# Kernel optimization log

Measured on AMD Instinct MI355X. Metric: run time of the kernel, lower is better.

The kernel has to match this reference:

```python
import math
import jax, jax.numpy as jnp
import numpy as np

NUM_BUCKETS = 32
MAX_DISTANCE = 128
N_HEADS = 16
D_KV = 64


def _relative_position_bucket(rel_pos):
    # encoder (bidirectional) path of UMT5Attention._relative_position_bucket
    num_buckets = NUM_BUCKETS // 2
    rel_buckets = (rel_pos > 0).astype(jnp.int32) * num_buckets
    rel_pos = jnp.abs(rel_pos)
    max_exact = num_buckets // 2
    is_small = rel_pos < max_exact
    # clamp to 1 inside log only to avoid nan; those entries are masked by is_small
    rel_pos_large = max_exact + (
        jnp.log(jnp.maximum(rel_pos, 1).astype(jnp.float32) / max_exact)
        / math.log(MAX_DISTANCE / max_exact)
        * (num_buckets - max_exact)
    ).astype(jnp.int32)
    rel_pos_large = jnp.minimum(rel_pos_large, num_buckets - 1)
    return rel_buckets + jnp.where(is_small, rel_pos, rel_pos_large)


def compute_bias(rel_bias, q_len, k_len):
    ctx = jnp.arange(q_len, dtype=jnp.int32)[:, None]
    mem = jnp.arange(k_len, dtype=jnp.int32)[None, :]
    bkt = _relative_position_bucket(mem - ctx)          # [q, k]
    values = rel_bias[bkt]                               # [q, k, H]
    return jnp.transpose(values, (2, 0, 1))[None]        # [1, H, q, k]


def setup_inputs() -> dict:
    key = jax.random.key(0)
    ks = jax.random.split(key, 6)
    B, S, D = 2, 2048, 1024
    s = 1.0 / math.sqrt(D)
    return {
        "hidden_states": jax.random.normal(ks[0], (B, S, D), jnp.float32),
        "attention_mask": jnp.ones((B, S), jnp.int32),
        "Wq": jax.random.normal(ks[1], (D, D), jnp.float32) * s,
        "Wk": jax.random.normal(ks[2], (D, D), jnp.float32) * s,
        "Wv": jax.random.normal(ks[3], (D, D), jnp.float32) * s,
        "Wo": jax.random.normal(ks[4], (D, D), jnp.float32) * s,
        "rel_bias": jax.random.normal(ks[5], (NUM_BUCKETS, N_HEADS), jnp.float32),
    }


def reference(hidden_states, attention_mask, Wq, Wk, Wv, Wo, rel_bias):
    b, s, _ = hidden_states.shape
    n, c = N_HEADS, D_KV
    q = (hidden_states @ Wq).reshape(b, s, n, c)
    k = (hidden_states @ Wk).reshape(b, s, n, c)
    v = (hidden_states @ Wv).reshape(b, s, n, c)
    position_bias = compute_bias(rel_bias, s, s)          # [1, H, s, s]
    mask = attention_mask[:, None, None, :]               # [b, 1, 1, s]
    position_bias = jnp.where(mask == 0,
                              jnp.finfo(hidden_states.dtype).min,
                              position_bias)
    # T5-style: no 1/sqrt(d) query scaling
    attn = jnp.einsum('binc,bjnc->bnij', q, k) + position_bias
    attn = jax.nn.softmax(attn, axis=-1)
    o = jnp.einsum('bnij,bjnc->binc', attn, v).reshape(b, s, n * c)
    return o @ Wo
```

## Files before the change

### kernel.cpp

```cpp
#include <hip/hip_runtime.h>
#include <hip/hip_bf16.h>

#define NH 16
#define DC 64
#define SEQ 2048
#define BATCH 2
#define DM 1024
#define MTOT (BATCH*SEQ)

#define LOG2E 1.44269504f
#define SMAX_BOUND 48.0f

typedef unsigned short u16;
typedef unsigned int u32;
typedef __bf16 bf16x8 __attribute__((ext_vector_type(8)));
typedef float f32x4 __attribute__((ext_vector_type(4)));
typedef int i32x4 __attribute__((ext_vector_type(4)));
typedef unsigned u32x2v __attribute__((ext_vector_type(2)));

struct __attribute__((packed, aligned(4))) f4u { f32x4 v; };

__device__ __forceinline__ u16 f2bf(float f) {
    unsigned int x = __float_as_uint(f);
    unsigned int r = (x + 0x7fffu + ((x >> 16) & 1u)) >> 16;
    return (u16)r;
}
__device__ __forceinline__ u32 cvtpk(float a, float b) {
    u32 r;
    asm("v_cvt_pk_bf16_f32 %0, %1, %2" : "=v"(r) : "v"(a), "v"(b));
    return r;
}

__device__ __forceinline__ float fexp2(float x) {
#if __has_builtin(__builtin_amdgcn_exp2f)
    return __builtin_amdgcn_exp2f(x);
#else
    return exp2f(x);
#endif
}

__device__ __forceinline__ f32x4 mfma16(bf16x8 a, bf16x8 b, f32x4 c) {
    return __builtin_amdgcn_mfma_f32_16x16x32_bf16(a, b, c, 0, 0, 0);
}

__device__ __forceinline__ void glds(const u16* g, u16* l) {
    __builtin_amdgcn_global_load_lds(
        (const __attribute__((address_space(1))) void*)g,
        (__attribute__((address_space(3))) void*)l, 16, 0, 0);
}

__device__ __forceinline__ float psum32(float v) {
    u32x2v t = __builtin_amdgcn_permlane32_swap(__float_as_uint(v), __float_as_uint(v), false, false);
    return __uint_as_float(t.x) + __uint_as_float(t.y);
}
__device__ __forceinline__ float psum16(float v) {
    u32x2v t = __builtin_amdgcn_permlane16_swap(__float_as_uint(v), __float_as_uint(v), false, false);
    return __uint_as_float(t.x) + __uint_as_float(t.y);
}


__global__ __launch_bounds__(256) void prep_kernel(
    const float* __restrict__ hs,
    const float* __restrict__ Wq, const float* __restrict__ Wk,
    const float* __restrict__ Wv, const float* __restrict__ Wo,
    const float* __restrict__ rel_bias,
    u16* __restrict__ hsb, u16* __restrict__ wT, float* __restrict__ btab)
{
    int bid = blockIdx.x, tid = threadIdx.x;
    if (bid < 4096) {
        int z = bid >> 10, rem = bid & 1023;
        int by = rem >> 5, bx = rem & 31;
        const float* W = (z == 0) ? Wq : (z == 1) ? Wk : (z == 2) ? Wv : Wo;
        float sc = (z == 0) ? LOG2E : 1.0f;
        u16* WT = wT + (size_t)z * DM * DM;
        __shared__ float tile[32][33];
        int tx = tid & 31, ty = tid >> 5;
        int kbase = by * 32, nbase = bx * 32;
#pragma unroll
        for (int i = 0; i < 4; i++)
            tile[ty * 4 + i][tx] = W[(size_t)(kbase + ty * 4 + i) * DM + nbase + tx];
        __syncthreads();
#pragma unroll
        for (int i = 0; i < 4; i++)
            WT[(size_t)(nbase + ty * 4 + i) * DM + kbase + tx] = f2bf(tile[tx][ty * 4 + i] * sc);
    } else if (bid < 6144) {
        int idx = (bid - 4096) * 256 + tid;
        int stride = 2048 * 256;
        int n4 = MTOT * DM / 4;
        for (int i = idx; i < n4; i += stride) {
            float4 v = reinterpret_cast<const float4*>(hs)[i];
            uint2 o;
            o.x = (unsigned)f2bf(v.x) | ((unsigned)f2bf(v.y) << 16);
            o.y = (unsigned)f2bf(v.z) | ((unsigned)f2bf(v.w) << 16);
            reinterpret_cast<uint2*>(hsb)[i] = o;
        }
    } else {
        int idx = (bid - 6144) * 256 + tid;
        int n = idx >> 12;
        int dpos = idx & 4095;
        int delta = dpos - 2048;
        int rb = (delta > 0) ? 16 : 0;
        int a = (delta < 0) ? -delta : delta;
        int ib;
        if (a < 8) {
            ib = a;
        } else {
            ib = 8 + (int)(logf((float)a / 8.0f) / logf(16.0f) * 8.0f);
            if (ib > 15) ib = 15;
        }
        btab[idx] = (rel_bias[(rb + ib) * NH + n] - SMAX_BOUND) * LOG2E;
    }
}

__global__ __launch_bounds__(256) void vtrans(const u16* __restrict__ V, u16* __restrict__ VT) {
    int st = blockIdx.x;
    int hb = blockIdx.y;
    const u16* src = V + ((size_t)hb * SEQ + st * 64) * DC;
    u16* dst = VT + (size_t)hb * DC * SEQ + st * 64;
    __shared__ u16 t[64][65];
    int tid = threadIdx.x;
    int r = tid >> 2, c0 = (tid & 3) * 16;
    union { bf16x8 v; u16 s[8]; } a0, a1;
    a0.v = *reinterpret_cast<const bf16x8*>(src + (size_t)r * DC + c0);
    a1.v = *reinterpret_cast<const bf16x8*>(src + (size_t)r * DC + c0 + 8);
#pragma unroll
    for (int j = 0; j < 8; j++) { t[r][c0 + j] = a0.s[j]; t[r][c0 + 8 + j] = a1.s[j]; }
    __syncthreads();
    int c = tid >> 2, s0 = (tid & 3) * 16;
    union { bf16x8 v; u16 s[8]; } o0, o1;
#pragma unroll
    for (int j = 0; j < 8; j++) { o0.s[j] = t[s0 + j][c]; o1.s[j] = t[s0 + 8 + j][c]; }
    *reinterpret_cast<bf16x8*>(dst + (size_t)c * SEQ + s0)     = o0.v;
    *reinterpret_cast<bf16x8*>(dst + (size_t)c * SEQ + s0 + 8) = o1.v;
}


template<int MODE>
__global__ __launch_bounds__(256) void gemm_bt(
    const u16* __restrict__ A, const u16* __restrict__ BT,
    u16* __restrict__ qkvout, float* __restrict__ fout)
{
    const int NTILES = DM / 128;
    const int MTILES = MTOT / 128;
    __shared__ u16 As[128 * 32];
    __shared__ u16 Bs[128 * 32];

    int nb8 = gridDim.x >> 3;
    int bid = (blockIdx.x & 7) * nb8 + (blockIdx.x >> 3);

    int proj = 0, mt, nt;
    if (MODE == 0) {
        proj = bid / (MTILES * NTILES);
        int r = bid % (MTILES * NTILES);
        mt = r / NTILES; nt = r % NTILES;
    } else {
        mt = bid / NTILES; nt = bid % NTILES;
    }
    const u16* Bp = BT + (size_t)proj * DM * DM;
    int m0 = mt * 128, n0 = nt * 128;
    int tid = threadIdx.x;
    int lane = tid & 63, wid = tid >> 6;
    int wrow = (wid >> 1) * 64, wcol = (wid & 1) * 64;

    f32x4 acc[4][4] = {};

    int srow = lane >> 2;
    int skoff = (lane & 3) * 8;

    for (int k0 = 0; k0 < DM; k0 += 32) {
        __syncthreads();
#pragma unroll
        for (int t = 0; t < 2; t++) {
            int chunk = wid * 2 + t;
            int row = chunk * 16 + srow;
            glds(A + (size_t)(m0 + row) * DM + k0 + skoff, &As[chunk * 512]);
        }
#pragma unroll
        for (int t = 0; t < 2; t++) {
            int chunk = wid * 2 + t;
            int row = chunk * 16 + srow;
            glds(Bp + (size_t)(n0 + row) * DM + k0 + skoff, &Bs[chunk * 512]);
        }
        __syncthreads();

        int ko = (lane >> 4) * 8;
        bf16x8 af[4], bfr[4];
#pragma unroll
        for (int mi = 0; mi < 4; mi++)
            af[mi] = *reinterpret_cast<const bf16x8*>(&As[(wrow + mi * 16 + (lane & 15)) * 32 + ko]);
#pragma unroll
        for (int ni = 0; ni < 4; ni++)
            bfr[ni] = *reinterpret_cast<const bf16x8*>(&Bs[(wcol + ni * 16 + (lane & 15)) * 32 + ko]);
#pragma unroll
        for (int mi = 0; mi < 4; mi++)
#pragma unroll
            for (int ni = 0; ni < 4; ni++)
                acc[mi][ni] = mfma16(af[mi], bfr[ni], acc[mi][ni]);
    }

    int rbase = (lane >> 4) * 4;
    int cidx = lane & 15;
#pragma unroll
    for (int mi = 0; mi < 4; mi++) {
#pragma unroll
        for (int ni = 0; ni < 4; ni++) {
#pragma unroll
            for (int r = 0; r < 4; r++) {
                int gm = m0 + wrow + mi * 16 + rbase + r;
                int gn = n0 + wcol + ni * 16 + cidx;
                float v = acc[mi][ni][r];
                if (MODE == 0) {
                    int b = gm >> 11, s = gm & (SEQ - 1);
                    int h = gn >> 6, c = gn & 63;
                    size_t off = (((size_t)b * NH + h) * SEQ + s) * DC + c;
                    qkvout[(size_t)proj * MTOT * DM + off] = f2bf(v);
                } else {
                    fout[(size_t)gm * DM + gn] = v;
                }
            }
        }
    }
}


__global__ __launch_bounds__(512, 4) void attn_kernel(
    const u16* __restrict__ Q, const u16* __restrict__ K, const u16* __restrict__ VT,
    const int* __restrict__ mask, const float* __restrict__ btab,
    u16* __restrict__ O)
{
    __shared__ u16 smem[32768];
    __shared__ float lds_l[4][2][16];

    int wg = blockIdx.x;
    int sw = (wg & 7) * 64 + (wg >> 3);
    int qt = sw & 15;
    int bh = sw >> 4;
    int h = bh & 15, b = bh >> 4;

    int tid = threadIdx.x, lane = tid & 63, wid = tid >> 6;
    int q15 = lane & 15, hi = lane >> 4;
    int qg = wid >> 1, kh = wid & 1;

    const u16* Qp  = Q  + (((size_t)b * NH + h) * SEQ) * DC;
    const u16* Kp  = K  + (((size_t)b * NH + h) * SEQ) * DC;
    const u16* VTp = VT + ((size_t)b * NH + h) * DC * SEQ;

    int qb = qt * 128 + qg * 32;
    int iq0 = qb + q15;
    int iq1 = qb + 16 + q15;

    bf16x8 qf00 = *reinterpret_cast<const bf16x8*>(Qp + (size_t)iq0 * DC + hi * 8);
    bf16x8 qf01 = *reinterpret_cast<const bf16x8*>(Qp + (size_t)iq0 * DC + 32 + hi * 8);
    bf16x8 qf10 = *reinterpret_cast<const bf16x8*>(Qp + (size_t)iq1 * DC + hi * 8);
    bf16x8 qf11 = *reinterpret_cast<const bf16x8*>(Qp + (size_t)iq1 * DC + 32 + hi * 8);

    int c0 = wid * 2, c1 = wid * 2 + 1;
    int lr0 = (c0 & 7) * 8 + (lane >> 3);
    int lr1 = (c1 & 7) * 8 + (lane >> 3);
    int cc0 = (lane & 7) ^ (lr0 & 7);
    int cc1 = (lane & 7) ^ (lr1 & 7);
    const u16* g0 = (wid < 4) ? (Kp + (size_t)lr0 * DC + cc0 * 8)
                              : (VTp + (size_t)lr0 * SEQ + cc0 * 8);
    const u16* g1 = (wid < 4) ? (Kp + (size_t)lr1 * DC + cc1 * 8)
                              : (VTp + (size_t)lr1 * SEQ + cc1 * 8);
    int adv = (wid < 4) ? 64 * DC : 64;

    int x0 = (hi)         ^ (q15 & 7);
    int x1 = (hi + 4)     ^ (q15 & 7);
    int xv = (kh * 4 + hi) ^ (q15 & 7);

    const float* bp0 = btab + (size_t)h * 2 * SEQ + 2048 + kh * 32 + hi * 4 - iq0;
    const float* bp1 = bp0 - 16;
    const int* mkp = mask + (size_t)b * SEQ + kh * 32 + hi * 4;

    f32x4 lv0 = {}, lv1 = {};
    f32x4 oacc[4][2] = {};

    glds(g0, &smem[c0 * 512]);
    glds(g1, &smem[c1 * 512]);
    const u16* pg0 = g0 + adv;
    const u16* pg1 = g1 + adv;

#pragma unroll 2
    for (int t = 0; t < SEQ / 64; t++) {
        u16* KsT = smem + ((t & 3) << 13);
        u16* VsT = KsT + 4096;
        int kt = t * 64;

        f32x4 bvm0[2], bvm1[2];
#pragma unroll
        for (int kf = 0; kf < 2; kf++) {
            f32x4 bv0 = reinterpret_cast<const f4u*>(bp0 + kt + kf * 16)->v;
            f32x4 bv1 = reinterpret_cast<const f4u*>(bp1 + kt + kf * 16)->v;
            i32x4 mv4 = *reinterpret_cast<const i32x4*>(mkp + kt + kf * 16);
#pragma unroll
            for (int r = 0; r < 4; r++) {
                bool mv = (mv4[r] != 0);
                bvm0[kf][r] = mv ? bv0[r] : -1e30f;
                bvm1[kf][r] = mv ? bv1[r] : -1e30f;
            }
        }

        if (t < SEQ / 64 - 1) {
            u16* nb = smem + (((t + 1) & 3) << 13);
            glds(pg0, &nb[c0 * 512]);
            glds(pg1, &nb[c1 * 512]);
            pg0 += adv;
            pg1 += adv;
            asm volatile("s_waitcnt vmcnt(2)" ::: "memory");
        } else {
            asm volatile("s_waitcnt vmcnt(0)" ::: "memory");
        }
        asm volatile("s_barrier" ::: "memory");

        f32x4 s0[2], s1[2];
        __builtin_amdgcn_s_setprio(1);
#pragma unroll
        for (int kf = 0; kf < 2; kf++) {
            int row = ((kh * 2 + kf) * 16 + q15) * 64;
            bf16x8 ka0 = *reinterpret_cast<const bf16x8*>(&KsT[row + x0 * 8]);
            bf16x8 ka1 = *reinterpret_cast<const bf16x8*>(&KsT[row + x1 * 8]);
            f32x4 z0 = bvm0[kf];
            z0 = mfma16(ka0, qf00, z0);
            z0 = mfma16(ka1, qf01, z0);
            s0[kf] = z0;
            f32x4 z1 = bvm1[kf];
            z1 = mfma16(ka0, qf10, z1);
            z1 = mfma16(ka1, qf11, z1);
            s1[kf] = z1;
        }
        __builtin_amdgcn_s_setprio(0);

#pragma unroll
        for (int kf = 0; kf < 2; kf++) {
#pragma unroll
            for (int r = 0; r < 4; r++) {
                s0[kf][r] = fexp2(s0[kf][r]);
                s1[kf][r] = fexp2(s1[kf][r]);
            }
            lv0 += s0[kf];
            lv1 += s1[kf];
        }

        bf16x8 pa0, pa1;
        {
            u32 cA0 = cvtpk(s0[0][0], s0[0][1]);
            u32 cA1 = cvtpk(s0[0][2], s0[0][3]);
            u32 cB0 = cvtpk(s0[1][0], s0[1][1]);
            u32 cB1 = cvtpk(s0[1][2], s0[1][3]);
            u32x2v t0 = __builtin_amdgcn_permlane32_swap(cA0, cB0, false, false);
            u32x2v t1 = __builtin_amdgcn_permlane32_swap(cA1, cB1, false, false);
            u32x2v t2 = __builtin_amdgcn_permlane16_swap(t0.x, t0.y, false, false);
            u32x2v t3 = __builtin_amdgcn_permlane16_swap(t1.x, t1.y, false, false);
            union { u32 w[4]; bf16x8 v; } up;
            up.w[0] = t2.x; up.w[1] = t3.x; up.w[2] = t2.y; up.w[3] = t3.y;
            pa0 = up.v;
        }
        {
            u32 cA0 = cvtpk(s1[0][0], s1[0][1]);
            u32 cA1 = cvtpk(s1[0][2], s1[0][3]);
            u32 cB0 = cvtpk(s1[1][0], s1[1][1]);
            u32 cB1 = cvtpk(s1[1][2], s1[1][3]);
            u32x2v t0 = __builtin_amdgcn_permlane32_swap(cA0, cB0, false, false);
            u32x2v t1 = __builtin_amdgcn_permlane32_swap(cA1, cB1, false, false);
            u32x2v t2 = __builtin_amdgcn_permlane16_swap(t0.x, t0.y, false, false);
            u32x2v t3 = __builtin_amdgcn_permlane16_swap(t1.x, t1.y, false, false);
            union { u32 w[4]; bf16x8 v; } up;
            up.w[0] = t2.x; up.w[1] = t3.x; up.w[2] = t2.y; up.w[3] = t3.y;
            pa1 = up.v;
        }

        __builtin_amdgcn_s_setprio(1);
#pragma unroll
        for (int ci = 0; ci < 4; ci++) {
            bf16x8 vf = *reinterpret_cast<const bf16x8*>(&VsT[(ci * 16 + q15) * 64 + xv * 8]);
            oacc[ci][0] = mfma16(vf, pa0, oacc[ci][0]);
            oacc[ci][1] = mfma16(vf, pa1, oacc[ci][1]);
        }
        __builtin_amdgcn_s_setprio(0);
    }

    float l0 = (lv0[0] + lv0[1]) + (lv0[2] + lv0[3]);
    float l1 = (lv1[0] + lv1[1]) + (lv1[2] + lv1[3]);
    l0 = psum16(psum32(l0));
    l1 = psum16(psum32(l1));
    __syncthreads();

    float* fs = reinterpret_cast<float*>(smem);
    if (kh == 1) {
#pragma unroll
        for (int ci = 0; ci < 4; ci++)
#pragma unroll
            for (int qs = 0; qs < 2; qs++)
                *reinterpret_cast<f32x4*>(&fs[qg * 2048 + (ci * 2 + qs) * 256 + lane * 4]) = oacc[ci][qs];
        if (hi == 0) { lds_l[qg][0][q15] = l0; lds_l[qg][1][q15] = l1; }
    }
    __syncthreads();

    float rl0 = 0.0f, rl1 = 0.0f;
    if (kh == 0) {
#pragma unroll
        for (int ci = 0; ci < 4; ci++)
#pragma unroll
            for (int qs = 0; qs < 2; qs++)
                oacc[ci][qs] += *reinterpret_cast<const f32x4*>(&fs[qg * 2048 + (ci * 2 + qs) * 256 + lane * 4]);
        rl0 = 1.0f / (l0 + lds_l[qg][0][q15]);
        rl1 = 1.0f / (l1 + lds_l[qg][1][q15]);
    }
    __syncthreads();

    u16* Ot = smem;
    if (kh == 0) {
#pragma unroll
        for (int ci = 0; ci < 4; ci++) {
            u32 w00 = cvtpk(oacc[ci][0][0] * rl0, oacc[ci][0][1] * rl0);
            u32 w01 = cvtpk(oacc[ci][0][2] * rl0, oacc[ci][0][3] * rl0);
            int base0 = (qg * 32 + q15) * 72 + ci * 16 + hi * 4;
            *reinterpret_cast<u32*>(&Ot[base0])     = w00;
            *reinterpret_cast<u32*>(&Ot[base0 + 2]) = w01;
            u32 w10 = cvtpk(oacc[ci][1][0] * rl1, oacc[ci][1][1] * rl1);
            u32 w11 = cvtpk(oacc[ci][1][2] * rl1, oacc[ci][1][3] * rl1);
            int base1 = (qg * 32 + 16 + q15) * 72 + ci * 16 + hi * 4;
            *reinterpret_cast<u32*>(&Ot[base1])     = w10;
            *reinterpret_cast<u32*>(&Ot[base1 + 2]) = w11;
        }
    }
    __syncthreads();
    int row = tid >> 2, part = tid & 3;
    bf16x8 o0 = *reinterpret_cast<const bf16x8*>(&Ot[row * 72 + part * 16]);
    bf16x8 o1 = *reinterpret_cast<const bf16x8*>(&Ot[row * 72 + part * 16 + 8]);
    size_t ob = ((size_t)b * SEQ + qt * 128 + row) * DM + h * DC + part * 16;
    *reinterpret_cast<bf16x8*>(&O[ob])     = o0;
    *reinterpret_cast<bf16x8*>(&O[ob + 8]) = o1;
}


extern "C" void kernel_launch(void* const* d_in, const int* in_sizes, int n_in,
                              void* d_out, int out_size, void* d_ws, size_t ws_size,
                              hipStream_t stream) {
    const float* hs   = (const float*)d_in[0];
    const int*   mask = (const int*)d_in[1];
    const float* Wq   = (const float*)d_in[2];
    const float* Wk   = (const float*)d_in[3];
    const float* Wv   = (const float*)d_in[4];
    const float* Wo   = (const float*)d_in[5];
    const float* rb   = (const float*)d_in[6];

    char* ws = (char*)d_ws;
    u16* hsb  = (u16*)(ws);
    u16* wT   = (u16*)(ws + 8388608);
    u16* Qb   = (u16*)(ws + 16777216);
    u16* Ob   = (u16*)(ws + 41943040);
    float* btab = (float*)(ws + 50331648);
    float* out = (float*)d_out;

    u16* VT = hsb;

    prep_kernel<<<6400, 256, 0, stream>>>(hs, Wq, Wk, Wv, Wo, rb, hsb, wT, btab);
    gemm_bt<0><<<768, 256, 0, stream>>>(hsb, wT, Qb, nullptr);
    vtrans<<<dim3(32, 32), 256, 0, stream>>>(Qb + 2 * (size_t)MTOT * DM, VT);
    attn_kernel<<<512, 512, 0, stream>>>(
        Qb, Qb + (size_t)MTOT * DM, VT, mask, btab, Ob);
    gemm_bt<1><<<256, 256, 0, stream>>>(Ob, wT + 3 * (size_t)DM * DM, nullptr, out);
}
```

Baseline: 134.7 us.

## Process two 64-key subtiles per barrier with double-buffered 128-key stages

```diff
diff --git a/kernel.cpp b/kernel.cpp
--- a/kernel.cpp
+++ b/kernel.cpp
@@ -263,7 +263,8 @@
                               : (VTp + (size_t)lr0 * SEQ + cc0 * 8);
     const u16* g1 = (wid < 4) ? (Kp + (size_t)lr1 * DC + cc1 * 8)
                               : (VTp + (size_t)lr1 * SEQ + cc1 * 8);
-    int adv = (wid < 4) ? 64 * DC : 64;
+    int subadv = (wid < 4) ? 64 * DC : 64;
+    int bigadv = 2 * subadv;
 
     int x0 = (hi)         ^ (q15 & 7);
     int x1 = (hi + 4)     ^ (q15 & 7);
@@ -276,55 +277,20 @@
     f32x4 lv0 = {}, lv1 = {};
     f32x4 oacc[4][2] = {};
 
-    glds(g0, &smem[c0 * 512]);
-    glds(g1, &smem[c1 * 512]);
-    const u16* pg0 = g0 + adv;
-    const u16* pg1 = g1 + adv;
-
-#pragma unroll 2
-    for (int t = 0; t < SEQ / 64; t++) {
-        u16* KsT = smem + ((t & 3) << 13);
-        u16* VsT = KsT + 4096;
-        int kt = t * 64;
-
-        f32x4 bvm0[2], bvm1[2];
-#pragma unroll
-        for (int kf = 0; kf < 2; kf++) {
-            f32x4 bv0 = reinterpret_cast<const f4u*>(bp0 + kt + kf * 16)->v;
-            f32x4 bv1 = reinterpret_cast<const f4u*>(bp1 + kt + kf * 16)->v;
-            i32x4 mv4 = *reinterpret_cast<const i32x4*>(mkp + kt + kf * 16);
-#pragma unroll
-            for (int r = 0; r < 4; r++) {
-                bool mv = (mv4[r] != 0);
-                bvm0[kf][r] = mv ? bv0[r] : -1e30f;
-                bvm1[kf][r] = mv ? bv1[r] : -1e30f;
-            }
-        }
-
-        if (t < SEQ / 64 - 1) {
-            u16* nb = smem + (((t + 1) & 3) << 13);
-            glds(pg0, &nb[c0 * 512]);
-            glds(pg1, &nb[c1 * 512]);
-            pg0 += adv;
-            pg1 += adv;
-            asm volatile("s_waitcnt vmcnt(2)" ::: "memory");
-        } else {
-            asm volatile("s_waitcnt vmcnt(0)" ::: "memory");
-        }
-        asm volatile("s_barrier" ::: "memory");
-
+    auto subtile = [&](const u16* Kt, const u16* Vt,
+                       f32x4 b00, f32x4 b01, f32x4 b10, f32x4 b11) {
         f32x4 s0[2], s1[2];
         __builtin_amdgcn_s_setprio(1);
 #pragma unroll
         for (int kf = 0; kf < 2; kf++) {
             int row = ((kh * 2 + kf) * 16 + q15) * 64;
-            bf16x8 ka0 = *reinterpret_cast<const bf16x8*>(&KsT[row + x0 * 8]);
-            bf16x8 ka1 = *reinterpret_cast<const bf16x8*>(&KsT[row + x1 * 8]);
-            f32x4 z0 = bvm0[kf];
+            bf16x8 ka0 = *reinterpret_cast<const bf16x8*>(&Kt[row + x0 * 8]);
+            bf16x8 ka1 = *reinterpret_cast<const bf16x8*>(&Kt[row + x1 * 8]);
+            f32x4 z0 = (kf == 0) ? b00 : b01;
             z0 = mfma16(ka0, qf00, z0);
             z0 = mfma16(ka1, qf01, z0);
             s0[kf] = z0;
-            f32x4 z1 = bvm1[kf];
+            f32x4 z1 = (kf == 0) ? b10 : b11;
             z1 = mfma16(ka0, qf10, z1);
             z1 = mfma16(ka1, qf11, z1);
             s1[kf] = z1;
@@ -373,11 +339,76 @@
         __builtin_amdgcn_s_setprio(1);
 #pragma unroll
         for (int ci = 0; ci < 4; ci++) {
-            bf16x8 vf = *reinterpret_cast<const bf16x8*>(&VsT[(ci * 16 + q15) * 64 + xv * 8]);
+            bf16x8 vf = *reinterpret_cast<const bf16x8*>(&Vt[(ci * 16 + q15) * 64 + xv * 8]);
             oacc[ci][0] = mfma16(vf, pa0, oacc[ci][0]);
             oacc[ci][1] = mfma16(vf, pa1, oacc[ci][1]);
         }
         __builtin_amdgcn_s_setprio(0);
+    };
+
+    glds(g0, &smem[c0 * 512]);
+    glds(g1, &smem[c1 * 512]);
+    glds(g0 + subadv, &smem[8192 + c0 * 512]);
+    glds(g1 + subadv, &smem[8192 + c1 * 512]);
+    const u16* pg0 = g0 + bigadv;
+    const u16* pg1 = g1 + bigadv;
+
+#pragma unroll 2
+    for (int t = 0; t < SEQ / 128; t++) {
+        u16* buf = smem + ((t & 1) << 14);
+        int kt = t * 128;
+
+        f32x4 bA00, bA01, bA10, bA11, bB00, bB01, bB10, bB11;
+        {
+            f32x4 v;
+            i32x4 mA0 = *reinterpret_cast<const i32x4*>(mkp + kt);
+            i32x4 mA1 = *reinterpret_cast<const i32x4*>(mkp + kt + 16);
+            i32x4 mB0 = *reinterpret_cast<const i32x4*>(mkp + kt + 64);
+            i32x4 mB1 = *reinterpret_cast<const i32x4*>(mkp + kt + 80);
+            v = reinterpret_cast<const f4u*>(bp0 + kt)->v;
+#pragma unroll
+            for (int r = 0; r < 4; r++) bA00[r] = (mA0[r] != 0) ? v[r] : -1e30f;
+            v = reinterpret_cast<const f4u*>(bp0 + kt + 16)->v;
+#pragma unroll
+            for (int r = 0; r < 4; r++) bA01[r] = (mA1[r] != 0) ? v[r] : -1e30f;
+            v = reinterpret_cast<const f4u*>(bp1 + kt)->v;
+#pragma unroll
+            for (int r = 0; r < 4; r++) bA10[r] = (mA0[r] != 0) ? v[r] : -1e30f;
+            v = reinterpret_cast<const f4u*>(bp1 + kt + 16)->v;
+#pragma unroll
+            for (int r = 0; r < 4; r++) bA11[r] = (mA1[r] != 0) ? v[r] : -1e30f;
+            v = reinterpret_cast<const f4u*>(bp0 + kt + 64)->v;
+#pragma unroll
+            for (int r = 0; r < 4; r++) bB00[r] = (mB0[r] != 0) ? v[r] : -1e30f;
+            v = reinterpret_cast<const f4u*>(bp0 + kt + 80)->v;
+#pragma unroll
+            for (int r = 0; r < 4; r++) bB01[r] = (mB1[r] != 0) ? v[r] : -1e30f;
+            v = reinterpret_cast<const f4u*>(bp1 + kt + 64)->v;
+#pragma unroll
+            for (int r = 0; r < 4; r++) bB10[r] = (mB0[r] != 0) ? v[r] : -1e30f;
+            v = reinterpret_cast<const f4u*>(bp1 + kt + 80)->v;
+#pragma unroll
+            for (int r = 0; r < 4; r++) bB11[r] = (mB1[r] != 0) ? v[r] : -1e30f;
+        }
+
+        if (t < SEQ / 128 - 1) {
+            u16* nb = smem + (((t + 1) & 1) << 14);
+            glds(pg0, &nb[c0 * 512]);
+            glds(pg1, &nb[c1 * 512]);
+            glds(pg0 + subadv, &nb[8192 + c0 * 512]);
+            glds(pg1 + subadv, &nb[8192 + c1 * 512]);
+            pg0 += bigadv;
+            pg1 += bigadv;
+            asm volatile("s_waitcnt vmcnt(4)" ::: "memory");
+        } else {
+            asm volatile("s_waitcnt vmcnt(0)" ::: "memory");
+        }
+        asm volatile("s_barrier" ::: "memory");
+
+        subtile(buf,        buf + 4096,  bA00, bA01, bA10, bA11);
+        subtile(buf + 8192, buf + 12288, bB00, bB01, bB10, bB11);
+
+        asm volatile("s_barrier" ::: "memory");
     }
 
     float l0 = (lv0[0] + lv0[1]) + (lv0[2] + lv0[3]);
```

Result: slower. 183.8 us (+36.5%).
